# Kernel optimization log

Hardware: AMD Instinct MI355X
Metric: run time of the kernel (lower is better)

Reference implementation:

```python
import jax, jax.numpy as jnp
import numpy as np

N, E, D, H, T, R, K = 40000, 320000, 128, 4, 3, 5, 3
DK = D // H
SQRT_DK = float(np.sqrt(DK))

def _glorot(key, shape):
    lim = float(np.sqrt(6.0 / (shape[-2] + shape[-1])))
    return jax.random.uniform(key, shape, jnp.float32, -lim, lim)

def setup_inputs():
    ks = jax.random.split(jax.random.key(0), 16)
    return {
        "meta_xs": jax.random.normal(ks[0], (N, D), jnp.float32),
        "node_type": jax.random.randint(ks[1], (N,), 0, T),
        "edge_index": jax.random.randint(ks[2], (2, E), 0, N),
        "edge_type": jax.random.randint(ks[3], (E,), 0, R),
        "edge_time": jax.random.randint(ks[4], (E,), 0, 100),
        "q_w": _glorot(ks[5], (T, D, D)), "q_b": jnp.zeros((T, D), jnp.float32),
        "k_w": _glorot(ks[6], (T, D, D)), "k_b": jnp.zeros((T, D), jnp.float32),
        "v_w": _glorot(ks[7], (T, D, D)), "v_b": jnp.zeros((T, D), jnp.float32),
        "a_w": _glorot(ks[8], (T, D, D)), "a_b": jnp.zeros((T, D), jnp.float32),
        "rel_pri": jnp.ones((R, H), jnp.float32),
        "rel_att": _glorot(ks[9], (R, H, DK, DK)),
        "rel_msg": _glorot(ks[10], (R, H, DK, DK)),
        "WMk": _glorot(ks[11], (K, D, D)),
        "Wak": _glorot(ks[12], (K, D, D)),
        "Wq": _glorot(ks[13], (D, D)), "bq": jnp.zeros((D,), jnp.float32),
        "Wkl": _glorot(ks[14], (D, D)), "bkl": jnp.zeros((D,), jnp.float32),
        "skip": jnp.ones((T,), jnp.float32),
        "ln_g": jnp.ones((T, D), jnp.float32),
        "ln_b": jnp.zeros((T, D), jnp.float32),
    }

def _forward(meta_xs, q_w, q_b, k_w, k_b, v_w, v_b, a_w, a_b, rel_pri, rel_att,
             rel_msg, WMk, Wak, Wq, bq, Wkl, bkl, skip, ln_g, ln_b,
             node_type, edge_index, edge_type):
    src, tgt = edge_index[0], edge_index[1]
    ar = jnp.arange(N)

    def typed(x, W, b):  # per-node-type linear: equivalent to the type-masked loops
        all_t = jnp.einsum('ni,tio->tno', x, W)        # [T, N, D]
        return all_t[node_type, ar] + b[node_type]      # [N, D]

    qn = typed(meta_xs, q_w, q_b).reshape(N, H, DK)
    kn = typed(meta_xs, k_w, k_b).reshape(N, H, DK)
    vn = typed(meta_xs, v_w, v_b).reshape(N, H, DK)
    qe, ke, ve = qn[tgt], kn[src], vn[src]              # [E, H, DK]

    # relation-specific bmm, honoring per-relation dispatch without [E,H,DK,DK] gather
    kp = jnp.zeros_like(ke)
    vp = jnp.zeros_like(ve)
    for r in range(R):
        sel = (edge_type == r)[:, None, None]
        kp = jnp.where(sel, jnp.einsum('ehd,hdm->ehm', ke, rel_att[r]), kp)
        vp = jnp.where(sel, jnp.einsum('ehd,hdm->ehm', ve, rel_msg[r]), vp)

    logits = (qe * kp).sum(-1) * rel_pri[edge_type] / SQRT_DK   # [E, H]
    # segment softmax over incoming edges per target node (torch_geometric softmax)
    mx = jax.ops.segment_max(logits, tgt, num_segments=N)
    ex = jnp.exp(logits - mx[tgt])
    att = ex / (jax.ops.segment_sum(ex, tgt, num_segments=N)[tgt] + 1e-16)

    # power-moment expanded, attention-weighted messages: [K, E, D]
    msgs = jnp.stack([((vp ** (kk + 1)) * att[:, :, None]).reshape(E, D) for kk in range(K)])

    # faithful to original aggregate(): messages indexed by target node id (not edge id)
    agg = jnp.stack([jax.ops.segment_sum(msgs[kk][tgt], tgt, num_segments=N) for kk in range(K)])
    # faithful: only the last moment gets the signed K-th root (loop re-clones each iter)
    root = jnp.sign(agg[K - 1]) * (jnp.abs(agg[K - 1]) + 1e-18) ** (1.0 / K)
    aggm = agg.at[K - 1].set(root)
    aggm = jnp.einsum('knd,kde->kne', aggm, WMk)        # [K, N, D]

    qlin = meta_xs @ Wq + bq
    res = jnp.zeros((N, D), meta_xs.dtype)
    for kk in range(K):
        front = qlin @ Wak[kk]                          # [N, D]
        tail = aggm[kk] @ Wkl + bkl                     # [N, D]
        t = jax.nn.sigmoid((front * tail).sum(-1))      # [N]
        res = res + t[:, None] * aggm[kk]

    # update(): gelu -> per-type linear -> learned skip -> per-type LayerNorm
    h = jax.nn.gelu(res, approximate=False)
    trans = typed(h, a_w, a_b)
    alpha = jax.nn.sigmoid(skip)[node_type][:, None]
    y = trans * alpha + meta_xs * (1.0 - alpha)
    mu = y.mean(-1, keepdims=True)
    var = ((y - mu) ** 2).mean(-1, keepdims=True)
    y = (y - mu) / jnp.sqrt(var + 1e-5) * ln_g[node_type] + ln_b[node_type]
    return y

def reference(meta_xs, node_type, edge_index, edge_type, edge_time,
              q_w, q_b, k_w, k_b, v_w, v_b, a_w, a_b, rel_pri, rel_att, rel_msg,
              WMk, Wak, Wq, bq, Wkl, bkl, skip, ln_g, ln_b):
    return _forward(meta_xs, q_w, q_b, k_w, k_b, v_w, v_b, a_w, a_b, rel_pri,
                    rel_att, rel_msg, WMk, Wak, Wq, bq, Wkl, bkl, skip, ln_g, ln_b,
                    node_type, edge_index, edge_type)
```

## Files before the change

### kernel.cpp

```cpp
#include <hip/hip_runtime.h>

#define N_ 40000
#define E_ 320000
#define D_ 128
#define H_ 4
#define T_ 3
#define R_ 5

typedef unsigned short u16;
typedef float f32x4 __attribute__((ext_vector_type(4)));
typedef short s16x8 __attribute__((ext_vector_type(8)));

__device__ __forceinline__ float bf2f(u16 h){ return __uint_as_float(((unsigned)h)<<16); }
__device__ __forceinline__ u16 f2bf(float f){
  unsigned u = __float_as_uint(f);
  u += 0x7fffu + ((u>>16)&1u);
  return (u16)(u>>16);
}
__device__ __forceinline__ unsigned fmono(float f){
  unsigned u = __float_as_uint(f);
  return (u>>31) ? ~u : (u | 0x80000000u);
}
__device__ __forceinline__ float monof(unsigned u){
  return (u>>31) ? __uint_as_float(u & 0x7fffffffu) : __uint_as_float(~u);
}
__device__ __forceinline__ float ldx(const void* p, long i, int f32){
  return f32 ? ((const float*)p)[i] : bf2f(((const u16*)p)[i]);
}
__device__ __forceinline__ float wredsum(float v){
  #pragma unroll
  for (int m=32;m;m>>=1) v += __shfl_xor(v, m, 64);
  return v;
}
__device__ __forceinline__ void split2(float v0, float v1, unsigned& hp, unsigned& lp){
  unsigned b0 = __float_as_uint(v0), b1 = __float_as_uint(v1);
  unsigned h0 = b0 & 0xFFFF0000u,    h1 = b1 & 0xFFFF0000u;
  float r0 = v0 - __uint_as_float(h0);
  float r1 = v1 - __uint_as_float(h1);
  hp = (h0>>16) | h1;
  lp = (__float_as_uint(r0)>>16) | (__float_as_uint(r1) & 0xFFFF0000u);
}

#define W_QW 0
#define W_KW 49152
#define W_VW 98304
#define W_AW 147456
#define W_QB 196608
#define W_KB 196992
#define W_VB 197376
#define W_AB 197760
#define W_PRI 198144
#define W_RATT 198164
#define W_RMSG 218644
#define W_WMK 239124
#define W_WAK 288276
#define W_WQ 337428
#define W_BQ 353812
#define W_WKL 353940
#define W_BKL 370324
#define W_SKIP 370452
#define W_LNG 370455
#define W_LNB 370839
#define W_TOT 371223

#define WT_Q   0
#define WT_K   98304
#define WT_V   196608
#define WT_A   294912
#define WT_WQ  396328
#define WT_WMK 478248

#define OFF_FLAGS 0ul
#define OFF_WCF   512ul
#define OFF_NT32  1485824ul
#define OFF_EI32  1646080ul
#define OFF_ET32  4206592ul
#define OFF_PERM  5486592ul
#define OFF_PCNT  5648384ul
#define OFF_TVAL  5648896ul
#define OFF_NPERM 5730816ul
#define OFF_LOG   6288896ul
#define OFF_QN    12848896ul
#define OFF_KN    33328896ul
#define OFF_VN    53808896ul
#define OFF_QLIN  74288896ul
#define OFF_QTR   94768896ul

__global__ __launch_bounds__(256) void detect_kernel(
    const u16* __restrict__ xs, const int* __restrict__ nt, int* __restrict__ flags)
{
  __shared__ int sBig, sZero, sNz;
  int tid = threadIdx.x;
  if (tid==0){ sBig=0; sZero=0; sNz=0; }
  __syncthreads();
  int big=0, zc=0;
  for (int i=tid; i<1024; i+=256) {
    u16 v = xs[2*i];
    int e = (v>>7)&0xFF;
    big += (e >= 200);
    zc  += (v == 0);
  }
  int nz=0;
  for (int i=tid; i<1024; i+=256) nz += (nt[2*i+1] != 0);
  atomicAdd(&sBig, big); atomicAdd(&sZero, zc); atomicAdd(&sNz, nz);
  __syncthreads();
  if (tid==0) {
    flags[0] = (sBig > 64) || (sZero > 900);
    flags[1] = (sNz == 0);
  }
}

struct FPtrs { const void* p[20]; };
__global__ __launch_bounds__(256) void convf_kernel(
    const int* __restrict__ flags, FPtrs ptrs, float* __restrict__ wcf)
{
  const int start[21] = {0,49152,98304,147456,196608,196992,197376,197760,198144,
    198164,218644,239124,288276,337428,353812,353940,370324,370452,370455,370839,371223};
  int i = blockIdx.x*256 + threadIdx.x;
  if (i >= W_TOT) return;
  int arr = 0;
  #pragma unroll
  for (int a=1; a<20; ++a) arr += (i >= start[a]);
  int local = i - start[arr];
  wcf[i] = ldx(ptrs.p[arr], local, flags[0]);
}

__global__ __launch_bounds__(256) void idxconv_kernel(
    const int* __restrict__ flags,
    const int* __restrict__ nt, const int* __restrict__ ei, const int* __restrict__ et,
    int* __restrict__ nt32, int* __restrict__ ei32, int* __restrict__ et32)
{
  int i = blockIdx.x*256 + threadIdx.x;
  if (i >= 1000000) return;
  int w = flags[1] ? 2 : 1;
  if (i < 40000)        nt32[i] = nt[(long)i*w];
  else if (i < 680000)  { int j=i-40000;  ei32[j] = ei[(long)j*w]; }
  else                  { int j=i-680000; et32[j] = et[(long)j*w]; }
}

__global__ __launch_bounds__(256) void pinit_kernel(int* __restrict__ perm, int* __restrict__ pc){
  int i = blockIdx.x*256 + threadIdx.x;
  if (i < 40448) perm[i] = -1;
  if (i < 12) pc[i] = 0;
}
__global__ __launch_bounds__(256) void einit_kernel(int* __restrict__ nperm, int* __restrict__ pc2){
  int i = blockIdx.x*256 + threadIdx.x;
  if (i < 40320) nperm[i] = -1;
  if (i < 16) pc2[i] = 0;
}
__global__ __launch_bounds__(256) void cnt_kernel(
    const int* __restrict__ keys, int n, int ntypes, int* __restrict__ gcnt)
{
  __shared__ int lh[8];
  if (threadIdx.x < ntypes) lh[threadIdx.x] = 0;
  __syncthreads();
  int i = blockIdx.x*256 + threadIdx.x;
  if (i < n) atomicAdd(&lh[keys[i]], 1);
  __syncthreads();
  if (threadIdx.x < ntypes && lh[threadIdx.x])
    atomicAdd(&gcnt[threadIdx.x], lh[threadIdx.x]);
}
__global__ void pofs_kernel(int* __restrict__ pc){
  if (threadIdx.x==0 && blockIdx.x==0) {
    pc[8] = 0;
    pc[9] = (pc[0]+127)&~127;
    pc[10] = pc[9] + ((pc[1]+127)&~127);
  }
}
__global__ void eofs_kernel(int* __restrict__ pc2){
  if (threadIdx.x==0 && blockIdx.x==0) {
    pc2[10] = 0;
    #pragma unroll
    for (int r=1;r<R_;++r) pc2[10+r] = pc2[10+r-1] + ((pc2[r-1]+63)&~63);
  }
}
__global__ __launch_bounds__(256) void scat_kernel(
    const int* __restrict__ keys, int n, int ntypes,
    const int* __restrict__ ofs, int* __restrict__ fill, int* __restrict__ perm)
{
  __shared__ int lh[8];
  __shared__ int lbase[8];
  if (threadIdx.x < ntypes) lh[threadIdx.x] = 0;
  __syncthreads();
  int i = blockIdx.x*256 + threadIdx.x;
  int t = 0, rank = 0;
  bool ok = (i < n);
  if (ok) { t = keys[i]; rank = atomicAdd(&lh[t], 1); }
  __syncthreads();
  if (threadIdx.x < ntypes)
    lbase[threadIdx.x] = lh[threadIdx.x] ? atomicAdd(&fill[threadIdx.x], lh[threadIdx.x]) : 0;
  __syncthreads();
  if (ok) perm[ofs[t] + lbase[t] + rank] = i;
}

__global__ __launch_bounds__(256) void init_kernel(
    unsigned* __restrict__ mxkey, float* __restrict__ sumex, int* __restrict__ deg)
{
  int i = blockIdx.x*256 + threadIdx.x;
  mxkey[i] = fmono(-1e30f);
  sumex[i] = 0.f;
  if (i < N_) deg[i] = 0;
}

__global__ __launch_bounds__(256) void prepA_kernel(
    const float* __restrict__ wcf, float* __restrict__ raT)
{
  int i = blockIdx.x*256 + threadIdx.x;
  if (i >= 20480) return;
  int d = i & 31, m = (i>>5) & 31, rh = i >> 10;
  raT[i] = wcf[W_RATT + (rh*32 + d)*32 + m];
}

__global__ __launch_bounds__(128) void prepB_kernel(
    const float* __restrict__ wcf, float* __restrict__ MT, float* __restrict__ ck)
{
  int col = threadIdx.x, i = blockIdx.x, k = blockIdx.y;
  const float* wak = wcf + W_WAK + k*16384 + col*128;
  const float* wkl = wcf + W_WKL + i*128;
  float acc = 0.f, accC = 0.f;
  #pragma unroll 8
  for (int j=0;j<128;++j) {
    float a = wak[j];
    acc  += a * wkl[j];
    if (i==0) accC += a * wcf[W_BKL + j];
  }
  MT[k*16384 + i*128 + col] = acc;
  if (i==0) ck[k*128 + col] = accC;
}

struct TPtrs { const void* p[16]; int soff[16]; int doff[16]; };
__global__ __launch_bounds__(256) void prepT_kernel(
    TPtrs tp, const int* __restrict__ flags, int xmode, u16* __restrict__ dst)
{
  __shared__ float T[128][33];
  int m = blockIdx.y;
  int c0 = blockIdx.x * 32;
  int tid = threadIdx.x;
  int xf = xmode ? 1 : flags[0];
  const void* src = tp.p[m];
  long sb = tp.soff[m];
  {
    int k = tid >> 1, ch = (tid & 1) * 16;
    #pragma unroll
    for (int j=0;j<16;++j)
      T[k][ch+j] = ldx(src, sb + (long)k*128 + c0 + ch + j, xf);
  }
  __syncthreads();
  int col = tid >> 3, k0 = (tid & 7) * 16;
  unsigned hp[8], lp[8];
  #pragma unroll
  for (int j=0;j<8;++j)
    split2(T[k0+2*j][col], T[k0+2*j+1][col], hp[j], lp[j]);
  u16* dh = dst + tp.doff[m] + (long)(c0+col)*128 + k0;
  ((uint4*)dh)[0] = uint4{hp[0],hp[1],hp[2],hp[3]};
  ((uint4*)dh)[1] = uint4{hp[4],hp[5],hp[6],hp[7]};
  u16* dl = dh + 16384;
  ((uint4*)dl)[0] = uint4{lp[0],lp[1],lp[2],lp[3]};
  ((uint4*)dl)[1] = uint4{lp[4],lp[5],lp[6],lp[7]};
}

struct GC4 { const float* x[4]; int woff[4]; int boff[4]; int typed[4]; };
__global__ __launch_bounds__(256) void gemmt2_kernel(
    GC4 cfg, const int* __restrict__ flags, int xmode,
    const u16* __restrict__ Wt, const float* __restrict__ wcf,
    const int* __restrict__ perm, const int* __restrict__ nt,
    int dotmode, const float* __restrict__ qlin, const float* __restrict__ ck,
    int powmode, const float* __restrict__ sattp, int wmode,
    float* __restrict__ out, long yostride)
{
  __shared__ u16 Wh[4096], Wl[4096];
  __shared__ int ridx[128];
  __shared__ int tblk_s;
  int tid = threadIdx.x;
  int y = blockIdx.y;
  int row0 = blockIdx.x*128;
  if (tid < 128) {
    int rr = row0 + tid;
    int rg = perm ? perm[rr] : (rr < N_ ? rr : -1);
    ridx[tid] = rg;
    if (tid==0) tblk_s = (perm && nt && rg>=0) ? nt[rg] : 0;
  }
  __syncthreads();
  if (ridx[0] < 0) return;
  int tblk = cfg.typed[y] ? tblk_s : 0;
  const u16* Wg = Wt + cfg.woff[y] + tblk*32768;
  const void* X = (const void*)cfg.x[y];
  int xf = xmode ? 1 : flags[0];
  int wlo_on = wmode ? 1 : flags[0];

  int lane = tid & 63;
  int wv   = tid >> 6;
  int lrow = lane & 15;
  int lk   = (lane >> 4) << 3;
  int rbase = wv*32;

  int sr0i = ridx[rbase + lrow];
  int sr1i = ridx[rbase + lrow + 16];
  long s0 = (sr0i < 0) ? 0 : (long)sr0i;
  long s1 = (sr1i < 0) ? 0 : (long)sr1i;

  int sr = tid >> 1;
  int sh = (tid & 1) * 16;
  int sp  = (sr >> 1) & 3;
  int sc0 = (sh >> 3) ^ sp;
  int sc1 = ((sh >> 3) + 1) ^ sp;

  f32x4 acc[2][8];
  #pragma unroll
  for (int m=0;m<2;++m)
    #pragma unroll
    for (int n=0;n<8;++n) acc[m][n] = f32x4{0.f,0.f,0.f,0.f};

  float4 fa0, fa1, fb0, fb1;
  uint4  ua = {0,0,0,0}, ub = {0,0,0,0};
  float  scp0 = 0.f, scp1 = 0.f;
  uint4  pw0, pw1, pw2 = {0,0,0,0}, pw3 = {0,0,0,0};

  if (xf) {
    const float4* x0 = reinterpret_cast<const float4*>((const float*)X + s0*128 + lk);
    const float4* x1 = reinterpret_cast<const float4*>((const float*)X + s1*128 + lk);
    fa0=x0[0]; fa1=x0[1]; fb0=x1[0]; fb1=x1[1];
    if (powmode) { scp0 = sattp[s0*4]; scp1 = sattp[s1*4]; }
  } else {
    ua = *reinterpret_cast<const uint4*>((const u16*)X + s0*128 + lk);
    ub = *reinterpret_cast<const uint4*>((const u16*)X + s1*128 + lk);
  }
  {
    const u16* gh = Wg + sr*128 + sh;
    pw0 = ((const uint4*)gh)[0]; pw1 = ((const uint4*)gh)[1];
    if (wlo_on) { pw2 = ((const uint4*)(gh+16384))[0]; pw3 = ((const uint4*)(gh+16384))[1]; }
  }

  for (int kc=0;kc<4;++kc) {
    s16x8 ah0, ah1, al0, al1;
    if (xf) {
      float t0[8] = {fa0.x,fa0.y,fa0.z,fa0.w, fa1.x,fa1.y,fa1.z,fa1.w};
      float t1[8] = {fb0.x,fb0.y,fb0.z,fb0.w, fb1.x,fb1.y,fb1.z,fb1.w};
      if (powmode) {
        #pragma unroll
        for (int j=0;j<8;++j) {
          float v0 = t0[j], v1 = t1[j];
          if (y==0)      { t0[j] = v0*scp0;    t1[j] = v1*scp1; }
          else if (y==1) { t0[j] = v0*v0*scp0; t1[j] = v1*v1*scp1; }
          else {
            float a3 = v0*v0*v0*scp0, b3 = v1*v1*v1*scp1;
            t0[j] = (a3==0.f) ? 0.f : copysignf(cbrtf(fabsf(a3)+1e-18f), a3);
            t1[j] = (b3==0.f) ? 0.f : copysignf(cbrtf(fabsf(b3)+1e-18f), b3);
          }
        }
      }
      unsigned h0[4], l0[4], h1[4], l1[4];
      #pragma unroll
      for (int j=0;j<4;++j) {
        split2(t0[2*j], t0[2*j+1], h0[j], l0[j]);
        split2(t1[2*j], t1[2*j+1], h1[j], l1[j]);
      }
      uint4 H0{h0[0],h0[1],h0[2],h0[3]}, L0{l0[0],l0[1],l0[2],l0[3]};
      uint4 H1{h1[0],h1[1],h1[2],h1[3]}, L1{l1[0],l1[1],l1[2],l1[3]};
      ah0 = *reinterpret_cast<s16x8*>(&H0); al0 = *reinterpret_cast<s16x8*>(&L0);
      ah1 = *reinterpret_cast<s16x8*>(&H1); al1 = *reinterpret_cast<s16x8*>(&L1);
    } else {
      ah0 = *reinterpret_cast<s16x8*>(&ua);
      ah1 = *reinterpret_cast<s16x8*>(&ub);
    }
    uint4 WH0 = pw0, WH1 = pw1, WL0 = pw2, WL1 = pw3;

    __syncthreads();
    ((uint4*)Wh)[sr*4 + sc0] = WH0;
    ((uint4*)Wh)[sr*4 + sc1] = WH1;
    if (wlo_on) {
      ((uint4*)Wl)[sr*4 + sc0] = WL0;
      ((uint4*)Wl)[sr*4 + sc1] = WL1;
    }
    if (kc < 3) {
      int kn_ = kc + 1;
      if (xf) {
        const float4* x0 = reinterpret_cast<const float4*>((const float*)X + s0*128 + kn_*32 + lk);
        const float4* x1 = reinterpret_cast<const float4*>((const float*)X + s1*128 + kn_*32 + lk);
        fa0=x0[0]; fa1=x0[1]; fb0=x1[0]; fb1=x1[1];
        if (powmode) { scp0 = sattp[s0*4 + kn_]; scp1 = sattp[s1*4 + kn_]; }
      } else {
        ua = *reinterpret_cast<const uint4*>((const u16*)X + s0*128 + kn_*32 + lk);
        ub = *reinterpret_cast<const uint4*>((const u16*)X + s1*128 + kn_*32 + lk);
      }
      const u16* gh = Wg + sr*128 + kn_*32 + sh;
      pw0 = ((const uint4*)gh)[0]; pw1 = ((const uint4*)gh)[1];
      if (wlo_on) { pw2 = ((const uint4*)(gh+16384))[0]; pw3 = ((const uint4*)(gh+16384))[1]; }
    }
    __syncthreads();
    #pragma unroll
    for (int n=0;n<8;++n) {
      int col = n*16 + lrow;
      int ib = col*32 + (lk ^ (((col>>1)&3)<<3));
      s16x8 bh = *(const s16x8*)(Wh + ib);
      acc[0][n] = __builtin_amdgcn_mfma_f32_16x16x32_bf16(ah0, bh, acc[0][n], 0,0,0);
      acc[1][n] = __builtin_amdgcn_mfma_f32_16x16x32_bf16(ah1, bh, acc[1][n], 0,0,0);
      if (xf) {
        acc[0][n] = __builtin_amdgcn_mfma_f32_16x16x32_bf16(al0, bh, acc[0][n], 0,0,0);
        acc[1][n] = __builtin_amdgcn_mfma_f32_16x16x32_bf16(al1, bh, acc[1][n], 0,0,0);
      }
      if (wlo_on) {
        s16x8 bl = *(const s16x8*)(Wl + ib);
        acc[0][n] = __builtin_amdgcn_mfma_f32_16x16x32_bf16(ah0, bl, acc[0][n], 0,0,0);
        acc[1][n] = __builtin_amdgcn_mfma_f32_16x16x32_bf16(ah1, bl, acc[1][n], 0,0,0);
      }
    }
  }

  int rq = (lane >> 4) << 2;
  if (!dotmode) {
    float b[8];
    if (cfg.boff[y] >= 0) {
      const float* bp = wcf + cfg.boff[y] + tblk*128;
      #pragma unroll
      for (int n=0;n<8;++n) b[n] = bp[n*16 + lrow];
    } else {
      #pragma unroll
      for (int n=0;n<8;++n) b[n] = 0.f;
    }
    #pragma unroll
    for (int m=0;m<2;++m) {
      #pragma unroll
      for (int r=0;r<4;++r) {
        int rowl = rbase + m*16 + rq + r;
        int rowg = ridx[rowl];
        if (rowg < 0) continue;
        float* op = out + (long)y*yostride + (long)rowg*128 + lrow;
        #pragma unroll
        for (int n=0;n<8;++n) op[n*16] = acc[m][n][r] + b[n];
      }
    }
  } else {
    float ckv[8];
    #pragma unroll
    for (int n=0;n<8;++n) ckv[n] = ck[y*128 + n*16 + lrow];
    #pragma unroll
    for (int m=0;m<2;++m) {
      #pragma unroll
      for (int r=0;r<4;++r) {
        int rowl = rbase + m*16 + rq + r;
        int rowg = ridx[rowl];
        float d = 0.f;
        if (rowg >= 0) {
          const float* qp = qlin + (long)rowg*128 + lrow;
          #pragma unroll
          for (int n=0;n<8;++n) d += (acc[m][n][r] + ckv[n]) * qp[n*16];
        }
        #pragma unroll
        for (int msk=1; msk<16; msk<<=1) d += __shfl_xor(d, msk, 64);
        if (lrow==0 && rowg>=0) out[(long)rowg*4 + y] = 1.f/(1.f+expf(-d));
      }
    }
  }
}

__global__ __launch_bounds__(256) void gemmbd_kernel(
    const float* __restrict__ X,
    const float* __restrict__ Wtab, int wsel,
    const int* __restrict__ perm, const int* __restrict__ gsrc, const int* __restrict__ et,
    float* __restrict__ out)
{
  __shared__ float As[64*152];
  __shared__ float Ws[4096];
  __shared__ int ridx[64];
  __shared__ int rsel_s;
  int tid = threadIdx.x;
  int row0 = blockIdx.x*64;
  if (tid < 64) {
    int rr = row0 + tid;
    int pe = perm ? perm[rr] : (rr < N_ ? rr : -1);
    ridx[tid] = pe;
    if (tid == 0) rsel_s = (wsel && pe >= 0) ? et[pe] : 0;
  }
  __syncthreads();
  if (ridx[0] < 0) return;
  const float* Wg = Wtab + (long)(wsel ? rsel_s : 0)*4096;
  #pragma unroll
  for (int j=0;j<4;++j)
    *reinterpret_cast<float4*>(&Ws[j*1024 + tid*4]) =
      *reinterpret_cast<const float4*>(Wg + j*1024 + tid*4);
  {
    int sar = tid >> 2, sh = tid & 3;
    int pe_s = ridx[sar];
    int arow = (pe_s < 0) ? -1 : (gsrc ? gsrc[pe_s] : pe_s);
    float* dst = &As[sar*152 + sh*36];
    if (arow < 0) {
      #pragma unroll
      for (int j=0;j<8;++j) *reinterpret_cast<float4*>(dst + j*4) = float4{0.f,0.f,0.f,0.f};
    } else {
      const float4* s4 = reinterpret_cast<const float4*>(X + (long)arow*128 + sh*32);
      #pragma unroll
      for (int j=0;j<8;++j) *reinterpret_cast<float4*>(dst + j*4) = s4[j];
    }
  }
  __syncthreads();
  int rg_ = tid >> 5, cg = tid & 31;
  int h = cg >> 3, c4 = (cg & 7)*4;
  float acc[8][4];
  #pragma unroll
  for (int r=0;r<8;++r){ acc[r][0]=0.f; acc[r][1]=0.f; acc[r][2]=0.f; acc[r][3]=0.f; }
  #pragma unroll
  for (int mq=0;mq<8;++mq) {
    float wv[4][4];
    #pragma unroll
    for (int i=0;i<4;++i) {
      float4 wt = *reinterpret_cast<const float4*>(&Ws[h*1024 + (mq*4+i)*32 + c4]);
      wv[i][0]=wt.x; wv[i][1]=wt.y; wv[i][2]=wt.z; wv[i][3]=wt.w;
    }
    #pragma unroll
    for (int r=0;r<8;++r) {
      float4 a4 = *reinterpret_cast<const float4*>(&As[(rg_*8+r)*152 + h*36 + mq*4]);
      float av[4] = {a4.x,a4.y,a4.z,a4.w};
      #pragma unroll
      for (int i=0;i<4;++i) {
        acc[r][0]+=av[i]*wv[i][0]; acc[r][1]+=av[i]*wv[i][1];
        acc[r][2]+=av[i]*wv[i][2]; acc[r][3]+=av[i]*wv[i][3];
      }
    }
  }
  #pragma unroll
  for (int r=0;r<8;++r) {
    int pe = ridx[rg_*8+r];
    if (pe < 0) continue;
    float4 o = {acc[r][0],acc[r][1],acc[r][2],acc[r][3]};
    *reinterpret_cast<float4*>(out + (long)pe*128 + h*32 + c4) = o;
  }
}

__global__ __launch_bounds__(256) void epass_kernel(
    const float* __restrict__ kn, const float* __restrict__ qtr, const float* __restrict__ wcf,
    const int* __restrict__ ei, const int* __restrict__ et, int rsel,
    float* __restrict__ logits, unsigned* __restrict__ mxkey, int* __restrict__ deg)
{
  int gid = blockIdx.x*256 + threadIdx.x;
  int e = gid >> 2, h = gid & 3;
  if (et[e] != rsel) return;
  int s = ei[e], t = ei[E_+e];
  const float4* ka = reinterpret_cast<const float4*>(kn + (long)s*128 + h*32);
  const float4* qa = reinterpret_cast<const float4*>(qtr + (long)t*128 + h*32);
  float acc = 0.f;
  #pragma unroll
  for (int i=0;i<8;++i) {
    float4 a = ka[i], b = qa[i];
    acc += a.x*b.x + a.y*b.y + a.z*b.z + a.w*b.w;
  }
  float lg = acc * wcf[W_PRI + rsel*H_+h] * 0.17677669529663687f;
  logits[gid] = lg;
  atomicMax(mxkey + t*H_+h, fmono(lg));
  if (h==0) atomicAdd(deg + t, 1);
}

__global__ __launch_bounds__(256) void eexp_kernel(
    const int* __restrict__ ei, float* __restrict__ logits,
    const unsigned* __restrict__ mxkey, float* __restrict__ sumex)
{
  int gid = blockIdx.x*256 + threadIdx.x;
  int e = gid >> 2, h = gid & 3;
  int t = ei[E_+e];
  float d = fminf(logits[gid] - monof(mxkey[t*H_+h]), 0.f);
  float ex = expf(d);
  if (e < N_) logits[gid] = ex;
  atomicAdd(sumex + t*H_+h, ex);
}

__global__ __launch_bounds__(256) void satt_kernel(
    const int* __restrict__ ei, const float* __restrict__ ex, const float* __restrict__ sumex,
    const int* __restrict__ deg, float* __restrict__ satt)
{
  int i = blockIdx.x*256 + threadIdx.x;
  int n = i >> 2, h = i & 3;
  int t = ei[E_+n];
  satt[i] = (float)deg[n] * ex[i] / (sumex[t*H_+h] + 1e-16f);
}

__global__ __launch_bounds__(256) void gatemix_kernel(
    const float* __restrict__ tval,
    const float* __restrict__ ag0, const float* __restrict__ ag1, const float* __restrict__ ag2,
    float* __restrict__ hout)
{
  long gid = (long)blockIdx.x*256 + threadIdx.x;
  int n = (int)(gid >> 7);
  float res = tval[n*4+0]*ag0[gid] + tval[n*4+1]*ag1[gid] + tval[n*4+2]*ag2[gid];
  hout[gid] = 0.5f*res*(1.f+erff(res*0.70710678118654752f));
}

__global__ __launch_bounds__(256) void lnf_kernel(
    const float* __restrict__ trans, const void* __restrict__ x, const int* __restrict__ flags,
    const int* __restrict__ nt, const float* __restrict__ wcf, void* __restrict__ outv)
{
  int wave = threadIdx.x >> 6, lane = threadIdx.x & 63;
  int n = blockIdx.x*4 + wave;
  int j = lane*2;
  int xf = flags[0];
  int t = nt[n];
  float alpha = 1.f/(1.f+expf(-wcf[W_SKIP+t]));
  long base = (long)n*128 + j;
  float y0 = alpha*trans[base]   + (1.f-alpha)*ldx(x, base,   xf);
  float y1 = alpha*trans[base+1] + (1.f-alpha)*ldx(x, base+1, xf);
  float mu = wredsum(y0+y1) * (1.f/128.f);
  float d0 = y0-mu, d1 = y1-mu;
  float var = wredsum(d0*d0+d1*d1) * (1.f/128.f);
  float inv = rsqrtf(var + 1e-5f);
  float o0 = d0*inv*wcf[W_LNG + t*128+j]   + wcf[W_LNB + t*128+j];
  float o1 = d1*inv*wcf[W_LNG + t*128+j+1] + wcf[W_LNB + t*128+j+1];
  if (xf) {
    ((float*)outv)[base]   = o0;
    ((float*)outv)[base+1] = o1;
  } else {
    unsigned o = (unsigned)f2bf(o0) | ((unsigned)f2bf(o1)<<16);
    *reinterpret_cast<unsigned*>(((u16*)outv)+base) = o;
  }
}

extern "C" void kernel_launch(void* const* d_in, const int* in_sizes, int n_in,
                              void* d_out, int out_size, void* d_ws, size_t ws_size,
                              hipStream_t stream) {
  char* w = (char*)d_ws;
  int*      flags = (int*)     (w + OFF_FLAGS);
  float*    wcf   = (float*)   (w + OFF_WCF);
  u16*      wtb   = (u16*)     (w + OFF_WCF);
  int*      nt32  = (int*)     (w + OFF_NT32);
  int*      ei32  = (int*)     (w + OFF_EI32);
  int*      et32  = (int*)     (w + OFF_ET32);
  int*      perm  = (int*)     (w + OFF_PERM);
  int*      pcnt  = (int*)     (w + OFF_PCNT);
  int*      pc2   = (int*)     (w + OFF_PCNT + 128);
  float*    raT   = (float*)   (w + OFF_TVAL);
  float*    satt  = (float*)   (w + OFF_TVAL);
  float*    tval  = (float*)   (w + OFF_TVAL);
  int*      nperm = (int*)     (w + OFF_NPERM);
  float*    logits= (float*)   (w + OFF_LOG);
  unsigned* mxkey = (unsigned*)(w + OFF_LOG + 5120000);
  float*    sumex = (float*)   (w + OFF_LOG + 5760000);
  int*      deg   = (int*)     (w + OFF_LOG + 6400000);
  float*    MT    = (float*)   (w + OFF_LOG);
  float*    ckb   = (float*)   (w + OFF_LOG + 786432);
  u16*      mtt   = (u16*)     (w + OFF_LOG + 1048576);
  float*    qn    = (float*)   (w + OFF_QN);
  float*    ag0   = (float*)   (w + OFF_QN);
  float*    trans = (float*)   (w + OFF_QN);
  float*    kn    = (float*)   (w + OFF_KN);
  float*    ag1   = (float*)   (w + OFF_KN);
  float*    vn    = (float*)   (w + OFF_VN);
  float*    ag2   = (float*)   (w + OFF_VN);
  float*    qlin  = (float*)   (w + OFF_QLIN);
  float*    hbuf  = (float*)   (w + OFF_QLIN);
  float*    qtrb  = (float*)   (w + OFF_QTR);
  float*    vp    = (float*)   (w + OFF_QTR);

  detect_kernel<<<1,256,0,stream>>>((const u16*)d_in[0], (const int*)d_in[1], flags);
  FPtrs fp;
  fp.p[0]=d_in[5];  fp.p[1]=d_in[7];  fp.p[2]=d_in[9];  fp.p[3]=d_in[11];
  fp.p[4]=d_in[6];  fp.p[5]=d_in[8];  fp.p[6]=d_in[10]; fp.p[7]=d_in[12];
  fp.p[8]=d_in[13]; fp.p[9]=d_in[14]; fp.p[10]=d_in[15];fp.p[11]=d_in[16];
  fp.p[12]=d_in[17];fp.p[13]=d_in[18];fp.p[14]=d_in[19];fp.p[15]=d_in[20];
  fp.p[16]=d_in[21];fp.p[17]=d_in[22];fp.p[18]=d_in[23];fp.p[19]=d_in[24];
  convf_kernel<<<1451,256,0,stream>>>(flags, fp, wcf);
  idxconv_kernel<<<3907,256,0,stream>>>(flags, (const int*)d_in[1],
                                        (const int*)d_in[2], (const int*)d_in[3],
                                        nt32, ei32, et32);
  pinit_kernel<<<159,256,0,stream>>>(perm, pcnt);
  cnt_kernel  <<<157,256,0,stream>>>(nt32, N_, T_, pcnt);
  pofs_kernel <<<1,64,0,stream>>>(pcnt);
  scat_kernel <<<157,256,0,stream>>>(nt32, N_, T_, pcnt+8, pcnt+4, perm);
  einit_kernel<<<158,256,0,stream>>>(nperm, pc2);
  cnt_kernel  <<<157,256,0,stream>>>(et32, N_, R_, pc2);
  eofs_kernel <<<1,64,0,stream>>>(pc2);
  scat_kernel <<<157,256,0,stream>>>(et32, N_, R_, pc2+10, pc2+5, nperm);
  prepA_kernel<<<80,256,0,stream>>>(wcf, raT);

  TPtrs tps;
  for (int t=0;t<3;++t) {
    tps.p[t]    = d_in[5];  tps.soff[t]    = t*16384; tps.doff[t]    = WT_Q   + t*32768;
    tps.p[3+t]  = d_in[7];  tps.soff[3+t]  = t*16384; tps.doff[3+t]  = WT_K   + t*32768;
    tps.p[6+t]  = d_in[9];  tps.soff[6+t]  = t*16384; tps.doff[6+t]  = WT_V   + t*32768;
    tps.p[9+t]  = d_in[11]; tps.soff[9+t]  = t*16384; tps.doff[9+t]  = WT_A   + t*32768;
    tps.p[13+t] = d_in[16]; tps.soff[13+t] = t*16384; tps.doff[13+t] = WT_WMK + t*32768;
  }
  tps.p[12] = d_in[18]; tps.soff[12] = 0; tps.doff[12] = WT_WQ;
  prepT_kernel<<<dim3(4,16),256,0,stream>>>(tps, flags, 0, wtb);

  GC4 cq;
  cq.x[0]=(const float*)d_in[0]; cq.x[1]=cq.x[0]; cq.x[2]=cq.x[0]; cq.x[3]=cq.x[0];
  cq.woff[0]=WT_Q; cq.woff[1]=WT_K; cq.woff[2]=WT_V; cq.woff[3]=WT_WQ;
  cq.boff[0]=W_QB; cq.boff[1]=W_KB; cq.boff[2]=W_VB; cq.boff[3]=W_BQ;
  cq.typed[0]=1; cq.typed[1]=1; cq.typed[2]=1; cq.typed[3]=0;
  gemmt2_kernel<<<dim3(316,4),256,0,stream>>>(cq, flags, 0, wtb, wcf, perm, nt32,
      0, nullptr, nullptr, 0, nullptr, 0, qn, 5120000);

  init_kernel<<<625,256,0,stream>>>(mxkey, sumex, deg);

  for (int r=0; r<R_; ++r) {
    gemmbd_kernel<<<625,256,0,stream>>>(qn, raT + r*4096, 0, nullptr, nullptr, nullptr, qtrb);
    epass_kernel<<<5000,256,0,stream>>>(kn, qtrb, wcf, ei32, et32, r, logits, mxkey, deg);
  }
  eexp_kernel<<<5000,256,0,stream>>>(ei32, logits, mxkey, sumex);

  gemmbd_kernel<<<630,256,0,stream>>>(vn, wcf+W_RMSG, 1, nperm, ei32, et32, vp);

  satt_kernel<<<625,256,0,stream>>>(ei32, logits, sumex, deg, satt);

  prepB_kernel<<<dim3(128,3),128,0,stream>>>(wcf, MT, ckb);
  TPtrs tpm;
  for (int i=0;i<16;++i){ tpm.p[i]=MT; tpm.soff[i]=0; tpm.doff[i]=0; }
  for (int k=0;k<3;++k){ tpm.soff[k]=k*16384; tpm.doff[k]=k*32768; }
  prepT_kernel<<<dim3(4,3),256,0,stream>>>(tpm, flags, 1, mtt);

  GC4 cp;
  cp.x[0]=vp; cp.x[1]=vp; cp.x[2]=vp; cp.x[3]=vp;
  cp.woff[0]=WT_WMK; cp.woff[1]=WT_WMK+32768; cp.woff[2]=WT_WMK+65536; cp.woff[3]=0;
  cp.boff[0]=-1; cp.boff[1]=-1; cp.boff[2]=-1; cp.boff[3]=-1;
  cp.typed[0]=0; cp.typed[1]=0; cp.typed[2]=0; cp.typed[3]=0;
  gemmt2_kernel<<<dim3(313,3),256,0,stream>>>(cp, flags, 1, wtb, wcf, nullptr, nullptr,
      0, nullptr, nullptr, 1, satt, 0, ag0, 5120000);

  GC4 cd;
  cd.x[0]=ag0; cd.x[1]=ag1; cd.x[2]=ag2; cd.x[3]=ag2;
  cd.woff[0]=0; cd.woff[1]=32768; cd.woff[2]=65536; cd.woff[3]=0;
  cd.boff[0]=-1; cd.boff[1]=-1; cd.boff[2]=-1; cd.boff[3]=-1;
  cd.typed[0]=0; cd.typed[1]=0; cd.typed[2]=0; cd.typed[3]=0;
  gemmt2_kernel<<<dim3(313,3),256,0,stream>>>(cd, flags, 1, mtt, wcf, nullptr, nullptr,
      1, qlin, ckb, 0, nullptr, 1, tval, 0);

  gatemix_kernel<<<20000,256,0,stream>>>(tval, ag0, ag1, ag2, hbuf);

  GC4 ct;
  ct.x[0]=hbuf; ct.x[1]=hbuf; ct.x[2]=hbuf; ct.x[3]=hbuf;
  ct.woff[0]=WT_A; ct.woff[1]=0; ct.woff[2]=0; ct.woff[3]=0;
  ct.boff[0]=W_AB; ct.boff[1]=-1; ct.boff[2]=-1; ct.boff[3]=-1;
  ct.typed[0]=1; ct.typed[1]=0; ct.typed[2]=0; ct.typed[3]=0;
  gemmt2_kernel<<<dim3(316,1),256,0,stream>>>(ct, flags, 1, wtb, wcf, perm, nt32,
      0, nullptr, nullptr, 0, nullptr, 0, trans, 0);

  lnf_kernel<<<10000,256,0,stream>>>(trans, d_in[0], flags, nt32, wcf, d_out);

  (void)in_sizes; (void)n_in; (void)out_size; (void)ws_size;
}
```

Before: 544.1 us.

## Preload full weight tile into LDS once instead of per-k-chunk staging

The GEMM kernel now loads the whole 128x128 bf16 weight (hi, and lo when enabled in one launch) into dynamically sized shared memory up front with an XOR swizzle. This removes the per-k-chunk double-sync staging loop. Where only the hi part is in LDS, the lo part is read straight from global memory. The cost is 32-64 KB of LDS per block, which may lower occupancy, and the weight load is no longer overlapped with compute.

```diff
diff --git a/kernel.cpp b/kernel.cpp
--- a/kernel.cpp
+++ b/kernel.cpp
@@ -265,10 +265,10 @@
     const u16* __restrict__ Wt, const float* __restrict__ wcf,
     const int* __restrict__ perm, const int* __restrict__ nt,
     int dotmode, const float* __restrict__ qlin, const float* __restrict__ ck,
-    int powmode, const float* __restrict__ sattp, int wmode,
+    int powmode, const float* __restrict__ sattp, int wmode, int wlds,
     float* __restrict__ out, long yostride)
 {
-  __shared__ u16 Wh[4096], Wl[4096];
+  extern __shared__ u16 smem[];
   __shared__ int ridx[128];
   __shared__ int tblk_s;
   int tid = threadIdx.x;
@@ -288,10 +288,31 @@
   int xf = xmode ? 1 : flags[0];
   int wlo_on = wmode ? 1 : flags[0];
 
+  {
+    int col = tid >> 1, half = tid & 1;
+    int key = col & 15;
+    #pragma unroll
+    for (int kc=0;kc<4;++kc) {
+      const uint4* gh = reinterpret_cast<const uint4*>(Wg + col*128 + kc*32 + half*16);
+      uint4 v0 = gh[0], v1 = gh[1];
+      int c0 = kc*4 + half*2;
+      ((uint4*)smem)[col*16 + (c0 ^ key)]       = v0;
+      ((uint4*)smem)[col*16 + ((c0+1) ^ key)]   = v1;
+      if (wlds && wlo_on) {
+        const uint4* gl = reinterpret_cast<const uint4*>(Wg + 16384 + col*128 + kc*32 + half*16);
+        uint4 w0 = gl[0], w1 = gl[1];
+        ((uint4*)(smem+16384))[col*16 + (c0 ^ key)]     = w0;
+        ((uint4*)(smem+16384))[col*16 + ((c0+1) ^ key)] = w1;
+      }
+    }
+  }
+  __syncthreads();
+
   int lane = tid & 63;
   int wv   = tid >> 6;
   int lrow = lane & 15;
-  int lk   = (lane >> 4) << 3;
+  int lkq  = lane >> 4;
+  int lk   = lkq << 3;
   int rbase = wv*32;
 
   int sr0i = ridx[rbase + lrow];
@@ -299,12 +320,6 @@
   long s0 = (sr0i < 0) ? 0 : (long)sr0i;
   long s1 = (sr1i < 0) ? 0 : (long)sr1i;
 
-  int sr = tid >> 1;
-  int sh = (tid & 1) * 16;
-  int sp  = (sr >> 1) & 3;
-  int sc0 = (sh >> 3) ^ sp;
-  int sc1 = ((sh >> 3) + 1) ^ sp;
-
   f32x4 acc[2][8];
   #pragma unroll
   for (int m=0;m<2;++m)
@@ -314,7 +329,6 @@
   float4 fa0, fa1, fb0, fb1;
   uint4  ua = {0,0,0,0}, ub = {0,0,0,0};
   float  scp0 = 0.f, scp1 = 0.f;
-  uint4  pw0, pw1, pw2 = {0,0,0,0}, pw3 = {0,0,0,0};
 
   if (xf) {
     const float4* x0 = reinterpret_cast<const float4*>((const float*)X + s0*128 + lk);
@@ -325,12 +339,8 @@
     ua = *reinterpret_cast<const uint4*>((const u16*)X + s0*128 + lk);
     ub = *reinterpret_cast<const uint4*>((const u16*)X + s1*128 + lk);
   }
-  {
-    const u16* gh = Wg + sr*128 + sh;
-    pw0 = ((const uint4*)gh)[0]; pw1 = ((const uint4*)gh)[1];
-    if (wlo_on) { pw2 = ((const uint4*)(gh+16384))[0]; pw3 = ((const uint4*)(gh+16384))[1]; }
-  }
-
+
+  #pragma unroll
   for (int kc=0;kc<4;++kc) {
     s16x8 ah0, ah1, al0, al1;
     if (xf) {
@@ -363,15 +373,6 @@
       ah0 = *reinterpret_cast<s16x8*>(&ua);
       ah1 = *reinterpret_cast<s16x8*>(&ub);
     }
-    uint4 WH0 = pw0, WH1 = pw1, WL0 = pw2, WL1 = pw3;
-
-    __syncthreads();
-    ((uint4*)Wh)[sr*4 + sc0] = WH0;
-    ((uint4*)Wh)[sr*4 + sc1] = WH1;
-    if (wlo_on) {
-      ((uint4*)Wl)[sr*4 + sc0] = WL0;
-      ((uint4*)Wl)[sr*4 + sc1] = WL1;
-    }
     if (kc < 3) {
       int kn_ = kc + 1;
       if (xf) {
@@ -383,16 +384,12 @@
         ua = *reinterpret_cast<const uint4*>((const u16*)X + s0*128 + kn_*32 + lk);
         ub = *reinterpret_cast<const uint4*>((const u16*)X + s1*128 + kn_*32 + lk);
       }
-      const u16* gh = Wg + sr*128 + kn_*32 + sh;
-      pw0 = ((const uint4*)gh)[0]; pw1 = ((const uint4*)gh)[1];
-      if (wlo_on) { pw2 = ((const uint4*)(gh+16384))[0]; pw3 = ((const uint4*)(gh+16384))[1]; }
-    }
-    __syncthreads();
+    }
     #pragma unroll
     for (int n=0;n<8;++n) {
       int col = n*16 + lrow;
-      int ib = col*32 + (lk ^ (((col>>1)&3)<<3));
-      s16x8 bh = *(const s16x8*)(Wh + ib);
+      int ibh = col*128 + (((kc*4 + lkq) ^ lrow) << 3);
+      s16x8 bh = *(const s16x8*)(smem + ibh);
       acc[0][n] = __builtin_amdgcn_mfma_f32_16x16x32_bf16(ah0, bh, acc[0][n], 0,0,0);
       acc[1][n] = __builtin_amdgcn_mfma_f32_16x16x32_bf16(ah1, bh, acc[1][n], 0,0,0);
       if (xf) {
@@ -400,14 +397,15 @@
         acc[1][n] = __builtin_amdgcn_mfma_f32_16x16x32_bf16(al1, bh, acc[1][n], 0,0,0);
       }
       if (wlo_on) {
-        s16x8 bl = *(const s16x8*)(Wl + ib);
+        s16x8 bl = wlds ? *(const s16x8*)(smem + 16384 + ibh)
+                        : *(const s16x8*)(Wg + 16384 + col*128 + kc*32 + lk);
         acc[0][n] = __builtin_amdgcn_mfma_f32_16x16x32_bf16(ah0, bl, acc[0][n], 0,0,0);
         acc[1][n] = __builtin_amdgcn_mfma_f32_16x16x32_bf16(ah1, bl, acc[1][n], 0,0,0);
       }
     }
   }
 
-  int rq = (lane >> 4) << 2;
+  int rq = lkq << 2;
   if (!dotmode) {
     float b[8];
     if (cfg.boff[y] >= 0) {
@@ -685,8 +683,8 @@
   cq.woff[0]=WT_Q; cq.woff[1]=WT_K; cq.woff[2]=WT_V; cq.woff[3]=WT_WQ;
   cq.boff[0]=W_QB; cq.boff[1]=W_KB; cq.boff[2]=W_VB; cq.boff[3]=W_BQ;
   cq.typed[0]=1; cq.typed[1]=1; cq.typed[2]=1; cq.typed[3]=0;
-  gemmt2_kernel<<<dim3(316,4),256,0,stream>>>(cq, flags, 0, wtb, wcf, perm, nt32,
-      0, nullptr, nullptr, 0, nullptr, 0, qn, 5120000);
+  gemmt2_kernel<<<dim3(316,4),256,32768,stream>>>(cq, flags, 0, wtb, wcf, perm, nt32,
+      0, nullptr, nullptr, 0, nullptr, 0, 0, qn, 5120000);
 
   init_kernel<<<625,256,0,stream>>>(mxkey, sumex, deg);
 
@@ -711,16 +709,16 @@
   cp.woff[0]=WT_WMK; cp.woff[1]=WT_WMK+32768; cp.woff[2]=WT_WMK+65536; cp.woff[3]=0;
   cp.boff[0]=-1; cp.boff[1]=-1; cp.boff[2]=-1; cp.boff[3]=-1;
   cp.typed[0]=0; cp.typed[1]=0; cp.typed[2]=0; cp.typed[3]=0;
-  gemmt2_kernel<<<dim3(313,3),256,0,stream>>>(cp, flags, 1, wtb, wcf, nullptr, nullptr,
-      0, nullptr, nullptr, 1, satt, 0, ag0, 5120000);
+  gemmt2_kernel<<<dim3(313,3),256,32768,stream>>>(cp, flags, 1, wtb, wcf, nullptr, nullptr,
+      0, nullptr, nullptr, 1, satt, 0, 0, ag0, 5120000);
 
   GC4 cd;
   cd.x[0]=ag0; cd.x[1]=ag1; cd.x[2]=ag2; cd.x[3]=ag2;
   cd.woff[0]=0; cd.woff[1]=32768; cd.woff[2]=65536; cd.woff[3]=0;
   cd.boff[0]=-1; cd.boff[1]=-1; cd.boff[2]=-1; cd.boff[3]=-1;
   cd.typed[0]=0; cd.typed[1]=0; cd.typed[2]=0; cd.typed[3]=0;
-  gemmt2_kernel<<<dim3(313,3),256,0,stream>>>(cd, flags, 1, mtt, wcf, nullptr, nullptr,
-      1, qlin, ckb, 0, nullptr, 1, tval, 0);
+  gemmt2_kernel<<<dim3(313,3),256,65536,stream>>>(cd, flags, 1, mtt, wcf, nullptr, nullptr,
+      1, qlin, ckb, 0, nullptr, 1, 1, tval, 0);
 
   gatemix_kernel<<<20000,256,0,stream>>>(tval, ag0, ag1, ag2, hbuf);
 
@@ -729,8 +727,8 @@
   ct.woff[0]=WT_A; ct.woff[1]=0; ct.woff[2]=0; ct.woff[3]=0;
   ct.boff[0]=W_AB; ct.boff[1]=-1; ct.boff[2]=-1; ct.boff[3]=-1;
   ct.typed[0]=1; ct.typed[1]=0; ct.typed[2]=0; ct.typed[3]=0;
-  gemmt2_kernel<<<dim3(316,1),256,0,stream>>>(ct, flags, 1, wtb, wcf, perm, nt32,
-      0, nullptr, nullptr, 0, nullptr, 0, trans, 0);
+  gemmt2_kernel<<<dim3(316,1),256,32768,stream>>>(ct, flags, 1, wtb, wcf, perm, nt32,
+      0, nullptr, nullptr, 0, nullptr, 0, 0, trans, 0);
 
   lnf_kernel<<<10000,256,0,stream>>>(trans, d_in[0], flags, nt32, wcf, d_out);
 
```

Result: slower. 613.8 us (+12.8%).
